# Performance work log

Hardware: AMD Instinct MI355X
Metric: run time of the kernel (lower is better)

## Reference

```python
import jax, jax.numpy as jnp
import numpy as np

H = 1024
V = 50257
L = 512


def setup_inputs() -> dict:
    key = jax.random.key(0)
    ks = jax.random.split(key, 12)
    s = 0.02
    return {
        "input_tok": jax.random.randint(ks[0], (1,), 0, V, dtype=jnp.int64),
        "hidden": jax.random.normal(ks[1], (1, 1, H), dtype=jnp.float32),
        "encoder_outputs": jax.random.normal(ks[2], (L, 1, H), dtype=jnp.float32),
        "embedding_w": jax.random.normal(ks[3], (V, H), dtype=jnp.float32) * s,
        "attn_combine_w": jax.random.normal(ks[4], (H, 2 * H), dtype=jnp.float32) * s,
        "attn_combine_b": jax.random.normal(ks[5], (H,), dtype=jnp.float32) * s,
        "w_ih": jax.random.normal(ks[6], (3 * H, H), dtype=jnp.float32) * s,
        "w_hh": jax.random.normal(ks[7], (3 * H, H), dtype=jnp.float32) * s,
        "b_ih": jax.random.normal(ks[8], (3 * H,), dtype=jnp.float32) * s,
        "b_hh": jax.random.normal(ks[9], (3 * H,), dtype=jnp.float32) * s,
        "out_w": jax.random.normal(ks[10], (V, H), dtype=jnp.float32) * s,
        "out_b": jax.random.normal(ks[11], (V,), dtype=jnp.float32) * s,
    }


def reference(input_tok, hidden, encoder_outputs, embedding_w,
              attn_combine_w, attn_combine_b, w_ih, w_hh, b_ih, b_hh,
              out_w, out_b):
    # embedding(input).view(1,1,-1); dropout is identity in eval mode
    embedded = embedding_w[input_tok[0]][None, :]          # [1, H]
    enc = encoder_outputs[:, 0, :]                          # [L, H]
    h0 = hidden[0]                                          # [1, H]
    # dot-product attention: hidden[0] @ enc^T
    attn_weights = jax.nn.softmax(h0 @ enc.T, axis=1)      # [1, L]
    attn_applied = attn_weights @ enc                       # [1, H]
    combined = jnp.concatenate([embedded, attn_applied], axis=1)  # [1, 2H]
    x = jax.nn.relu(combined @ attn_combine_w.T + attn_combine_b)  # [1, H]
    # single-step GRU cell (PyTorch gate ordering: r, z, n)
    gi = x @ w_ih.T + b_ih                                  # [1, 3H]
    gh = h0 @ w_hh.T + b_hh                                 # [1, 3H]
    r = jax.nn.sigmoid(gi[:, :H] + gh[:, :H])
    z = jax.nn.sigmoid(gi[:, H:2 * H] + gh[:, H:2 * H])
    n = jnp.tanh(gi[:, 2 * H:] + r * gh[:, 2 * H:])
    h_new = (1.0 - z) * n + z * h0                          # [1, H]
    logp = jax.nn.log_softmax(h_new @ out_w.T + out_b, axis=1)  # [1, V]
    return logp, h_new[None], attn_weights
```

## Files before the change

### kernel.cpp

```cpp
#include <hip/hip_runtime.h>
#include <math.h>

#define H  1024
#define H2 2048
#define H3 3072
#define V  50257
#define L  512

__device__ __forceinline__ float dot4(float4 a, float4 b) {
    return a.x*b.x + a.y*b.y + a.z*b.z + a.w*b.w;
}
__device__ __forceinline__ float wave_red_sum(float acc) {
    for (int off = 32; off > 0; off >>= 1) acc += __shfl_down(acc, off, 64);
    return acc;
}

__global__ void __launch_bounds__(256) k_pre(
        const float* __restrict__ h0, const float* __restrict__ enc,
        const float* __restrict__ w_hh, const float* __restrict__ b_hh,
        float* __restrict__ scores, float* __restrict__ gh) {
    __shared__ float s[4];
    int t = threadIdx.x, lane = t & 63, wv = t >> 6;
    if (blockIdx.x < 512) {
        int l = blockIdx.x;
        float4 a = ((const float4*)(enc + (size_t)l * H))[t];
        float4 b = ((const float4*)h0)[t];
        float acc = wave_red_sum(dot4(a, b));
        if (lane == 0) s[wv] = acc;
        __syncthreads();
        if (t == 0) scores[l] = s[0] + s[1] + s[2] + s[3];
    } else {
        int row = (blockIdx.x - 512) * 4 + wv;
        const float4* wr = (const float4*)(w_hh + (size_t)row * H);
        const float4* h4 = (const float4*)h0;
        float acc = 0.f;
        #pragma unroll
        for (int j = 0; j < 4; ++j) acc += dot4(wr[j * 64 + lane], h4[j * 64 + lane]);
        acc = wave_red_sum(acc);
        if (lane == 0) gh[row] = acc + b_hh[row];
    }
}

__global__ void __launch_bounds__(256) k_softmax_attn(
        const float* __restrict__ enc, const float* __restrict__ scores,
        float* __restrict__ attn_applied, float* __restrict__ d_out) {
    __shared__ float wl[L];
    __shared__ float red[256];
    __shared__ float part[8][32];
    int t = threadIdx.x;
    float s0 = scores[t], s1 = scores[t + 256];
    red[t] = fmaxf(s0, s1);
    __syncthreads();
    for (int off = 128; off > 0; off >>= 1) {
        if (t < off) red[t] = fmaxf(red[t], red[t + off]);
        __syncthreads();
    }
    float gmax = red[0];
    __syncthreads();
    float e0 = expf(s0 - gmax), e1 = expf(s1 - gmax);
    red[t] = e0 + e1;
    __syncthreads();
    for (int off = 128; off > 0; off >>= 1) {
        if (t < off) red[t] += red[t + off];
        __syncthreads();
    }
    float inv = 1.0f / red[0];
    wl[t]       = e0 * inv;
    wl[t + 256] = e1 * inv;
    __syncthreads();
    if (blockIdx.x == 0) {
        d_out[V + H + t]       = wl[t];
        d_out[V + H + t + 256] = wl[t + 256];
    }
    int c = t & 31, sIdx = t >> 5;
    int col = blockIdx.x * 32 + c;
    float acc = 0.f;
    for (int l = sIdx * 64; l < sIdx * 64 + 64; ++l)
        acc += wl[l] * enc[(size_t)l * H + col];
    part[sIdx][c] = acc;
    __syncthreads();
    if (sIdx == 0) {
        float sum = 0.f;
        #pragma unroll
        for (int k = 0; k < 8; ++k) sum += part[k][c];
        attn_applied[col] = sum;
    }
}

__global__ void __launch_bounds__(256) k_combine(
        const float* __restrict__ emb_w, const int* __restrict__ tok,
        const float* __restrict__ attn_applied, const float* __restrict__ Wc,
        const float* __restrict__ bc, float* __restrict__ x) {
    __shared__ float comb[H2];
    int t = threadIdx.x;
    int tk = tok[0];
    ((float4*)comb)[t]       = ((const float4*)(emb_w + (size_t)tk * H))[t];
    ((float4*)comb)[t + 256] = ((const float4*)attn_applied)[t];
    __syncthreads();
    int lane = t & 63, wv = t >> 6;
    int row = blockIdx.x * 4 + wv;
    const float4* wr = (const float4*)(Wc + (size_t)row * H2);
    float acc = 0.f;
    #pragma unroll
    for (int j = 0; j < 8; ++j) acc += dot4(wr[j * 64 + lane], ((const float4*)comb)[j * 64 + lane]);
    acc = wave_red_sum(acc);
    if (lane == 0) x[row] = fmaxf(acc + bc[row], 0.f);
}

__global__ void __launch_bounds__(256) k_gi_gru(
        const float* __restrict__ x, const float* __restrict__ h0,
        const float* __restrict__ w_ih, const float* __restrict__ b_ih,
        const float* __restrict__ gh, float* __restrict__ d_out,
        float* __restrict__ hnew) {
    int t = threadIdx.x, lane = t & 63, wv = t >> 6;
    int i = blockIdx.x * 4 + wv;
    const float4* xv = (const float4*)x;
    float g[3];
    #pragma unroll
    for (int k = 0; k < 3; ++k) {
        const float4* wr = (const float4*)(w_ih + (size_t)(k * H + i) * H);
        float acc = 0.f;
        #pragma unroll
        for (int j = 0; j < 4; ++j) acc += dot4(wr[j * 64 + lane], xv[j * 64 + lane]);
        g[k] = wave_red_sum(acc);
    }
    if (lane == 0) {
        float gir = g[0] + b_ih[i];
        float giz = g[1] + b_ih[H + i];
        float gin = g[2] + b_ih[2 * H + i];
        float r = 1.f / (1.f + expf(-(gir + gh[i])));
        float z = 1.f / (1.f + expf(-(giz + gh[H + i])));
        float n = tanhf(gin + r * gh[2 * H + i]);
        float h = (1.f - z) * n + z * h0[i];
        d_out[V + i] = h;
        hnew[i] = h;
    }
}

__global__ void __launch_bounds__(256) k_logits(
        const float* __restrict__ hnew, const float* __restrict__ out_w,
        const float* __restrict__ out_b, float* __restrict__ logits) {
    __shared__ float hs[H];
    int t = threadIdx.x;
    ((float4*)hs)[t] = ((const float4*)hnew)[t];
    __syncthreads();
    int lane = t & 63, wv = t >> 6;
    int row0 = (blockIdx.x * 4 + wv) * 2;
    if (row0 >= V) return;
    const float4* hs4 = (const float4*)hs;
    const float4* w0 = (const float4*)(out_w + (size_t)row0 * H);
    float acc0 = 0.f, acc1 = 0.f;
    if (row0 + 1 < V) {
        const float4* w1 = (const float4*)(out_w + (size_t)(row0 + 1) * H);
        #pragma unroll
        for (int j = 0; j < 4; ++j) {
            float4 b = hs4[j * 64 + lane];
            acc0 += dot4(w0[j * 64 + lane], b);
            acc1 += dot4(w1[j * 64 + lane], b);
        }
        for (int off = 32; off > 0; off >>= 1) {
            acc0 += __shfl_down(acc0, off, 64);
            acc1 += __shfl_down(acc1, off, 64);
        }
        if (lane == 0) {
            logits[row0]     = acc0 + out_b[row0];
            logits[row0 + 1] = acc1 + out_b[row0 + 1];
        }
    } else {
        #pragma unroll
        for (int j = 0; j < 4; ++j) acc0 += dot4(w0[j * 64 + lane], hs4[j * 64 + lane]);
        acc0 = wave_red_sum(acc0);
        if (lane == 0) logits[row0] = acc0 + out_b[row0];
    }
}

__global__ void __launch_bounds__(256) k_lse_part(
        const float* __restrict__ logits, float* __restrict__ pm,
        float* __restrict__ ps) {
    __shared__ float red[4];
    int b = blockIdx.x, t = threadIdx.x, lane = t & 63, wv = t >> 6;
    const int CH = (V + 63) / 64;
    int begin = b * CH;
    int end = begin + CH; if (end > V) end = V;
    float v[4]; int cnt = 0;
    for (int i = begin + t; i < end; i += 256) v[cnt++] = logits[i];
    float m = -INFINITY;
    for (int c = 0; c < cnt; ++c) m = fmaxf(m, v[c]);
    for (int off = 32; off > 0; off >>= 1) m = fmaxf(m, __shfl_down(m, off, 64));
    if (lane == 0) red[wv] = m;
    __syncthreads();
    float M = fmaxf(fmaxf(red[0], red[1]), fmaxf(red[2], red[3]));
    __syncthreads();
    float s = 0.f;
    for (int c = 0; c < cnt; ++c) s += expf(v[c] - M);
    s = wave_red_sum(s);
    if (lane == 0) red[wv] = s;
    __syncthreads();
    if (t == 0) {
        pm[b] = M;
        ps[b] = red[0] + red[1] + red[2] + red[3];
    }
}

__global__ void __launch_bounds__(256) k_logp(
        float* __restrict__ d_out, const float* __restrict__ pm,
        const float* __restrict__ ps) {
    __shared__ float sh[2];
    int t = threadIdx.x;
    if (t < 64) {
        float m = pm[t], s = ps[t];
        float M = m;
        for (int off = 32; off > 0; off >>= 1) M = fmaxf(M, __shfl_down(M, off, 64));
        M = __shfl(M, 0, 64);
        float sc = s * expf(m - M);
        sc = wave_red_sum(sc);
        if (t == 0) { sh[0] = M; sh[1] = logf(sc); }
    }
    __syncthreads();
    float M = sh[0], Ls = sh[1];
    int i = blockIdx.x * 256 + t;
    if (i < V) d_out[i] = d_out[i] - M - Ls;
}

extern "C" void kernel_launch(void* const* d_in, const int* in_sizes, int n_in,
                              void* d_out, int out_size, void* d_ws, size_t ws_size,
                              hipStream_t stream) {
    const int*   tok    = (const int*)d_in[0];
    const float* hidden = (const float*)d_in[1];
    const float* enc    = (const float*)d_in[2];
    const float* emb_w  = (const float*)d_in[3];
    const float* Wc     = (const float*)d_in[4];
    const float* bc     = (const float*)d_in[5];
    const float* w_ih   = (const float*)d_in[6];
    const float* w_hh   = (const float*)d_in[7];
    const float* b_ih   = (const float*)d_in[8];
    const float* b_hh   = (const float*)d_in[9];
    const float* out_w  = (const float*)d_in[10];
    const float* out_b  = (const float*)d_in[11];
    float* out = (float*)d_out;
    float* ws  = (float*)d_ws;

    float* scores       = ws;
    float* gh           = ws + 1024;
    float* attn_applied = ws + 4096;
    float* xbuf         = ws + 5120;
    float* hnew         = ws + 6144;
    float* pm           = ws + 7168;
    float* psum         = ws + 7232;

    k_pre         <<<1280, 256, 0, stream>>>(hidden, enc, w_hh, b_hh, scores, gh);
    k_softmax_attn<<<32,   256, 0, stream>>>(enc, scores, attn_applied, out);
    k_combine     <<<256,  256, 0, stream>>>(emb_w, tok, attn_applied, Wc, bc, xbuf);
    k_gi_gru      <<<256,  256, 0, stream>>>(xbuf, hidden, w_ih, b_ih, gh, out, hnew);
    k_logits      <<<(V + 7) / 8, 256, 0, stream>>>(hnew, out_w, out_b, out);
    k_lse_part    <<<64,   256, 0, stream>>>(out, pm, psum);
    k_logp        <<<(V + 255) / 256, 256, 0, stream>>>(out, pm, psum);
}
```

Before: 416.8 us.

## Fuse decoder step into one cooperative kernel with grid syncs and online logsumexp

Replaces the seven separate launches with a single cooperative kernel of 1024 blocks. The stages (scores and gh, softmax-attention, combine, GRU, logits, log-softmax) are separated by grid.sync() calls. Attention application is rewritten so each block reduces one column across all rows, and the logits stage folds the running max and sum into an online logsumexp, which removes the separate pass over the logits. The aim is to cut launch gaps and an extra read of the logits, at the price of five grid-wide barriers and fewer waves resident per CU during the large out_w GEMV.

```diff
diff --git a/kernel.cpp b/kernel.cpp
--- a/kernel.cpp
+++ b/kernel.cpp
@@ -1,225 +1,228 @@
 #include <hip/hip_runtime.h>
+#include <hip/hip_cooperative_groups.h>
 #include <math.h>
+
+namespace cg = cooperative_groups;
 
 #define H  1024
 #define H2 2048
-#define H3 3072
 #define V  50257
 #define L  512
+#define NB 1024
+#define NT 256
+#define NG ((V + 7) / 8)
 
 __device__ __forceinline__ float dot4(float4 a, float4 b) {
     return a.x*b.x + a.y*b.y + a.z*b.z + a.w*b.w;
 }
-__device__ __forceinline__ float wave_red_sum(float acc) {
-    for (int off = 32; off > 0; off >>= 1) acc += __shfl_down(acc, off, 64);
-    return acc;
-}
-
-__global__ void __launch_bounds__(256) k_pre(
-        const float* __restrict__ h0, const float* __restrict__ enc,
-        const float* __restrict__ w_hh, const float* __restrict__ b_hh,
-        float* __restrict__ scores, float* __restrict__ gh) {
-    __shared__ float s[4];
-    int t = threadIdx.x, lane = t & 63, wv = t >> 6;
-    if (blockIdx.x < 512) {
-        int l = blockIdx.x;
-        float4 a = ((const float4*)(enc + (size_t)l * H))[t];
-        float4 b = ((const float4*)h0)[t];
-        float acc = wave_red_sum(dot4(a, b));
-        if (lane == 0) s[wv] = acc;
-        __syncthreads();
-        if (t == 0) scores[l] = s[0] + s[1] + s[2] + s[3];
-    } else {
-        int row = (blockIdx.x - 512) * 4 + wv;
-        const float4* wr = (const float4*)(w_hh + (size_t)row * H);
-        const float4* h4 = (const float4*)h0;
-        float acc = 0.f;
+__device__ __forceinline__ float wave_red_sum(float v) {
+    #pragma unroll
+    for (int off = 32; off > 0; off >>= 1) v += __shfl_down(v, off, 64);
+    return v;
+}
+__device__ __forceinline__ float wave_red_max(float v) {
+    #pragma unroll
+    for (int off = 32; off > 0; off >>= 1) v = fmaxf(v, __shfl_down(v, off, 64));
+    return v;
+}
+
+__global__ void __launch_bounds__(NT, 4) k_fused(
+        const int* __restrict__ tok,   const float* __restrict__ h0,
+        const float* __restrict__ enc, const float* __restrict__ emb_w,
+        const float* __restrict__ Wc,  const float* __restrict__ bc,
+        const float* __restrict__ w_ih,const float* __restrict__ w_hh,
+        const float* __restrict__ b_ih,const float* __restrict__ b_hh,
+        const float* __restrict__ out_w,const float* __restrict__ out_b,
+        float* __restrict__ d_out,     float* __restrict__ ws)
+{
+    cg::grid_group grid = cg::this_grid();
+    __shared__ float4 sh4[512];
+    __shared__ float  sred[8];
+
+    float* scores = ws;
+    float* gh     = ws + 1024;
+    float* attn   = ws + 4096;
+    float* xv     = ws + 5120;
+    float* hnew   = ws + 6144;
+    float* pm     = ws + 7168;
+    float* ps     = ws + 8192;
+
+    const int t = threadIdx.x, lane = t & 63, wv = t >> 6;
+    const int b = blockIdx.x;
+
+    for (int it = b; it < 512 + 768; it += NB) {
+        if (it < 512) {
+            const float4* er = (const float4*)(enc + (size_t)it * H);
+            float acc = wave_red_sum(dot4(er[t], ((const float4*)h0)[t]));
+            if (lane == 0) sred[wv] = acc;
+            __syncthreads();
+            if (t == 0) scores[it] = sred[0] + sred[1] + sred[2] + sred[3];
+            __syncthreads();
+        } else {
+            int row = (it - 512) * 4 + wv;
+            const float4* wr = (const float4*)(w_hh + (size_t)row * H);
+            const float4* h4 = (const float4*)h0;
+            float acc = 0.f;
+            #pragma unroll
+            for (int j = 0; j < 4; ++j) acc += dot4(wr[j*64 + lane], h4[j*64 + lane]);
+            acc = wave_red_sum(acc);
+            if (lane == 0) gh[row] = acc + b_hh[row];
+        }
+    }
+    grid.sync();
+
+    {
+        float s0 = scores[t], s1 = scores[t + 256];
+        float m = wave_red_max(fmaxf(s0, s1));
+        if (lane == 0) sred[wv] = m;
+        __syncthreads();
+        float gmax = fmaxf(fmaxf(sred[0], sred[1]), fmaxf(sred[2], sred[3]));
+        __syncthreads();
+        float e0 = expf(s0 - gmax), e1 = expf(s1 - gmax);
+        float ssum = wave_red_sum(e0 + e1);
+        if (lane == 0) sred[wv] = ssum;
+        __syncthreads();
+        float inv = 1.f / (sred[0] + sred[1] + sred[2] + sred[3]);
+        __syncthreads();
+        float w0 = e0 * inv, w1 = e1 * inv;
+        if (b == 0) {
+            d_out[V + H + t]       = w0;
+            d_out[V + H + 256 + t] = w1;
+        }
+        float acc = w0 * enc[(size_t)t * H + b] + w1 * enc[(size_t)(t + 256) * H + b];
+        acc = wave_red_sum(acc);
+        if (lane == 0) sred[wv] = acc;
+        __syncthreads();
+        if (t == 0) attn[b] = sred[0] + sred[1] + sred[2] + sred[3];
+    }
+    grid.sync();
+
+    {
+        int tk = tok[0];
+        const float4* er = (const float4*)(emb_w + (size_t)tk * H);
+        sh4[t]       = er[t];
+        sh4[256 + t] = ((const float4*)attn)[t];
+        __syncthreads();
+        const float4* wr = (const float4*)(Wc + (size_t)b * H2);
+        float acc = dot4(wr[t], sh4[t]) + dot4(wr[256 + t], sh4[256 + t]);
+        acc = wave_red_sum(acc);
+        if (lane == 0) sred[wv] = acc;
+        __syncthreads();
+        if (t == 0) xv[b] = fmaxf(sred[0] + sred[1] + sred[2] + sred[3] + bc[b], 0.f);
+        __syncthreads();
+    }
+    grid.sync();
+
+    {
+        if (wv < 3) {
+            const float4* wr = (const float4*)(w_ih + (size_t)(wv * H + b) * H);
+            const float4* x4 = (const float4*)xv;
+            float acc = 0.f;
+            #pragma unroll
+            for (int j = 0; j < 4; ++j) acc += dot4(wr[j*64 + lane], x4[j*64 + lane]);
+            acc = wave_red_sum(acc);
+            if (lane == 0) sred[wv] = acc;
+        }
+        __syncthreads();
+        if (t == 0) {
+            float gir = sred[0] + b_ih[b];
+            float giz = sred[1] + b_ih[H + b];
+            float gin = sred[2] + b_ih[2 * H + b];
+            float r = 1.f / (1.f + expf(-(gir + gh[b])));
+            float z = 1.f / (1.f + expf(-(giz + gh[H + b])));
+            float n = tanhf(gin + r * gh[2 * H + b]);
+            float h = (1.f - z) * n + z * h0[b];
+            hnew[b] = h;
+            d_out[V + b] = h;
+        }
+    }
+    grid.sync();
+
+    {
+        sh4[t] = ((const float4*)hnew)[t];
+        __syncthreads();
+        float m_run = -INFINITY, s_run = 0.f;
+        for (int g = b; g < NG; g += NB) {
+            int r0 = g * 8 + wv * 2;
+            if (r0 + 1 < V) {
+                const float4* w0 = (const float4*)(out_w + (size_t)r0 * H);
+                const float4* w1 = w0 + 256;
+                float a0 = 0.f, a1 = 0.f;
+                #pragma unroll
+                for (int j = 0; j < 4; ++j) {
+                    float4 hv = sh4[j*64 + lane];
+                    a0 += dot4(w0[j*64 + lane], hv);
+                    a1 += dot4(w1[j*64 + lane], hv);
+                }
+                #pragma unroll
+                for (int off = 32; off > 0; off >>= 1) {
+                    a0 += __shfl_down(a0, off, 64);
+                    a1 += __shfl_down(a1, off, 64);
+                }
+                if (lane == 0) {
+                    float v0 = a0 + out_b[r0];
+                    float v1 = a1 + out_b[r0 + 1];
+                    d_out[r0]     = v0;
+                    d_out[r0 + 1] = v1;
+                    float mn = fmaxf(m_run, fmaxf(v0, v1));
+                    s_run = s_run * expf(m_run - mn) + expf(v0 - mn) + expf(v1 - mn);
+                    m_run = mn;
+                }
+            } else if (r0 < V) {
+                const float4* w0 = (const float4*)(out_w + (size_t)r0 * H);
+                float a0 = 0.f;
+                #pragma unroll
+                for (int j = 0; j < 4; ++j) a0 += dot4(w0[j*64 + lane], sh4[j*64 + lane]);
+                a0 = wave_red_sum(a0);
+                if (lane == 0) {
+                    float v0 = a0 + out_b[r0];
+                    d_out[r0] = v0;
+                    float mn = fmaxf(m_run, v0);
+                    s_run = s_run * expf(m_run - mn) + expf(v0 - mn);
+                    m_run = mn;
+                }
+            }
+        }
+        if (lane == 0) { sred[wv] = m_run; sred[4 + wv] = s_run; }
+        __syncthreads();
+        if (t == 0) {
+            float M = fmaxf(fmaxf(sred[0], sred[1]), fmaxf(sred[2], sred[3]));
+            float S = 0.f;
+            #pragma unroll
+            for (int k = 0; k < 4; ++k) S += sred[4 + k] * expf(sred[k] - M);
+            pm[b] = M; ps[b] = S;
+        }
+    }
+    grid.sync();
+
+    {
+        float m = -INFINITY, s = 0.f;
         #pragma unroll
-        for (int j = 0; j < 4; ++j) acc += dot4(wr[j * 64 + lane], h4[j * 64 + lane]);
-        acc = wave_red_sum(acc);
-        if (lane == 0) gh[row] = acc + b_hh[row];
-    }
-}
-
-__global__ void __launch_bounds__(256) k_softmax_attn(
-        const float* __restrict__ enc, const float* __restrict__ scores,
-        float* __restrict__ attn_applied, float* __restrict__ d_out) {
-    __shared__ float wl[L];
-    __shared__ float red[256];
-    __shared__ float part[8][32];
-    int t = threadIdx.x;
-    float s0 = scores[t], s1 = scores[t + 256];
-    red[t] = fmaxf(s0, s1);
-    __syncthreads();
-    for (int off = 128; off > 0; off >>= 1) {
-        if (t < off) red[t] = fmaxf(red[t], red[t + off]);
-        __syncthreads();
-    }
-    float gmax = red[0];
-    __syncthreads();
-    float e0 = expf(s0 - gmax), e1 = expf(s1 - gmax);
-    red[t] = e0 + e1;
-    __syncthreads();
-    for (int off = 128; off > 0; off >>= 1) {
-        if (t < off) red[t] += red[t + off];
-        __syncthreads();
-    }
-    float inv = 1.0f / red[0];
-    wl[t]       = e0 * inv;
-    wl[t + 256] = e1 * inv;
-    __syncthreads();
-    if (blockIdx.x == 0) {
-        d_out[V + H + t]       = wl[t];
-        d_out[V + H + t + 256] = wl[t + 256];
-    }
-    int c = t & 31, sIdx = t >> 5;
-    int col = blockIdx.x * 32 + c;
-    float acc = 0.f;
-    for (int l = sIdx * 64; l < sIdx * 64 + 64; ++l)
-        acc += wl[l] * enc[(size_t)l * H + col];
-    part[sIdx][c] = acc;
-    __syncthreads();
-    if (sIdx == 0) {
-        float sum = 0.f;
+        for (int k = 0; k < 4; ++k) {
+            int i = t * 4 + k;
+            float mi = pm[i], si = ps[i];
+            float mn = fmaxf(m, mi);
+            s = s * expf(m - mn) + si * expf(mi - mn);
+            m = mn;
+        }
         #pragma unroll
-        for (int k = 0; k < 8; ++k) sum += part[k][c];
-        attn_applied[col] = sum;
-    }
-}
-
-__global__ void __launch_bounds__(256) k_combine(
-        const float* __restrict__ emb_w, const int* __restrict__ tok,
-        const float* __restrict__ attn_applied, const float* __restrict__ Wc,
-        const float* __restrict__ bc, float* __restrict__ x) {
-    __shared__ float comb[H2];
-    int t = threadIdx.x;
-    int tk = tok[0];
-    ((float4*)comb)[t]       = ((const float4*)(emb_w + (size_t)tk * H))[t];
-    ((float4*)comb)[t + 256] = ((const float4*)attn_applied)[t];
-    __syncthreads();
-    int lane = t & 63, wv = t >> 6;
-    int row = blockIdx.x * 4 + wv;
-    const float4* wr = (const float4*)(Wc + (size_t)row * H2);
-    float acc = 0.f;
-    #pragma unroll
-    for (int j = 0; j < 8; ++j) acc += dot4(wr[j * 64 + lane], ((const float4*)comb)[j * 64 + lane]);
-    acc = wave_red_sum(acc);
-    if (lane == 0) x[row] = fmaxf(acc + bc[row], 0.f);
-}
-
-__global__ void __launch_bounds__(256) k_gi_gru(
-        const float* __restrict__ x, const float* __restrict__ h0,
-        const float* __restrict__ w_ih, const float* __restrict__ b_ih,
-        const float* __restrict__ gh, float* __restrict__ d_out,
-        float* __restrict__ hnew) {
-    int t = threadIdx.x, lane = t & 63, wv = t >> 6;
-    int i = blockIdx.x * 4 + wv;
-    const float4* xv = (const float4*)x;
-    float g[3];
-    #pragma unroll
-    for (int k = 0; k < 3; ++k) {
-        const float4* wr = (const float4*)(w_ih + (size_t)(k * H + i) * H);
-        float acc = 0.f;
+        for (int off = 32; off > 0; off >>= 1) {
+            float mo = __shfl_down(m, off, 64);
+            float so = __shfl_down(s, off, 64);
+            float mn = fmaxf(m, mo);
+            s = s * expf(m - mn) + so * expf(mo - mn);
+            m = mn;
+        }
+        if (lane == 0) { sred[wv] = m; sred[4 + wv] = s; }
+        __syncthreads();
+        float M = fmaxf(fmaxf(sred[0], sred[1]), fmaxf(sred[2], sred[3]));
+        float S = 0.f;
         #pragma unroll
-        for (int j = 0; j < 4; ++j) acc += dot4(wr[j * 64 + lane], xv[j * 64 + lane]);
-        g[k] = wave_red_sum(acc);
-    }
-    if (lane == 0) {
-        float gir = g[0] + b_ih[i];
-        float giz = g[1] + b_ih[H + i];
-        float gin = g[2] + b_ih[2 * H + i];
-        float r = 1.f / (1.f + expf(-(gir + gh[i])));
-        float z = 1.f / (1.f + expf(-(giz + gh[H + i])));
-        float n = tanhf(gin + r * gh[2 * H + i]);
-        float h = (1.f - z) * n + z * h0[i];
-        d_out[V + i] = h;
-        hnew[i] = h;
-    }
-}
-
-__global__ void __launch_bounds__(256) k_logits(
-        const float* __restrict__ hnew, const float* __restrict__ out_w,
-        const float* __restrict__ out_b, float* __restrict__ logits) {
-    __shared__ float hs[H];
-    int t = threadIdx.x;
-    ((float4*)hs)[t] = ((const float4*)hnew)[t];
-    __syncthreads();
-    int lane = t & 63, wv = t >> 6;
-    int row0 = (blockIdx.x * 4 + wv) * 2;
-    if (row0 >= V) return;
-    const float4* hs4 = (const float4*)hs;
-    const float4* w0 = (const float4*)(out_w + (size_t)row0 * H);
-    float acc0 = 0.f, acc1 = 0.f;
-    if (row0 + 1 < V) {
-        const float4* w1 = (const float4*)(out_w + (size_t)(row0 + 1) * H);
-        #pragma unroll
-        for (int j = 0; j < 4; ++j) {
-            float4 b = hs4[j * 64 + lane];
-            acc0 += dot4(w0[j * 64 + lane], b);
-            acc1 += dot4(w1[j * 64 + lane], b);
-        }
-        for (int off = 32; off > 0; off >>= 1) {
-            acc0 += __shfl_down(acc0, off, 64);
-            acc1 += __shfl_down(acc1, off, 64);
-        }
-        if (lane == 0) {
-            logits[row0]     = acc0 + out_b[row0];
-            logits[row0 + 1] = acc1 + out_b[row0 + 1];
-        }
-    } else {
-        #pragma unroll
-        for (int j = 0; j < 4; ++j) acc0 += dot4(w0[j * 64 + lane], hs4[j * 64 + lane]);
-        acc0 = wave_red_sum(acc0);
-        if (lane == 0) logits[row0] = acc0 + out_b[row0];
-    }
-}
-
-__global__ void __launch_bounds__(256) k_lse_part(
-        const float* __restrict__ logits, float* __restrict__ pm,
-        float* __restrict__ ps) {
-    __shared__ float red[4];
-    int b = blockIdx.x, t = threadIdx.x, lane = t & 63, wv = t >> 6;
-    const int CH = (V + 63) / 64;
-    int begin = b * CH;
-    int end = begin + CH; if (end > V) end = V;
-    float v[4]; int cnt = 0;
-    for (int i = begin + t; i < end; i += 256) v[cnt++] = logits[i];
-    float m = -INFINITY;
-    for (int c = 0; c < cnt; ++c) m = fmaxf(m, v[c]);
-    for (int off = 32; off > 0; off >>= 1) m = fmaxf(m, __shfl_down(m, off, 64));
-    if (lane == 0) red[wv] = m;
-    __syncthreads();
-    float M = fmaxf(fmaxf(red[0], red[1]), fmaxf(red[2], red[3]));
-    __syncthreads();
-    float s = 0.f;
-    for (int c = 0; c < cnt; ++c) s += expf(v[c] - M);
-    s = wave_red_sum(s);
-    if (lane == 0) red[wv] = s;
-    __syncthreads();
-    if (t == 0) {
-        pm[b] = M;
-        ps[b] = red[0] + red[1] + red[2] + red[3];
-    }
-}
-
-__global__ void __launch_bounds__(256) k_logp(
-        float* __restrict__ d_out, const float* __restrict__ pm,
-        const float* __restrict__ ps) {
-    __shared__ float sh[2];
-    int t = threadIdx.x;
-    if (t < 64) {
-        float m = pm[t], s = ps[t];
-        float M = m;
-        for (int off = 32; off > 0; off >>= 1) M = fmaxf(M, __shfl_down(M, off, 64));
-        M = __shfl(M, 0, 64);
-        float sc = s * expf(m - M);
-        sc = wave_red_sum(sc);
-        if (t == 0) { sh[0] = M; sh[1] = logf(sc); }
-    }
-    __syncthreads();
-    float M = sh[0], Ls = sh[1];
-    int i = blockIdx.x * 256 + t;
-    if (i < V) d_out[i] = d_out[i] - M - Ls;
+        for (int k = 0; k < 4; ++k) S += sred[4 + k] * expf(sred[k] - M);
+        float off = M + logf(S);
+        int i = b * NT + t;
+        if (i < V) d_out[i] -= off;
+    }
 }
 
 extern "C" void kernel_launch(void* const* d_in, const int* in_sizes, int n_in,
@@ -240,19 +243,9 @@
     float* out = (float*)d_out;
     float* ws  = (float*)d_ws;
 
-    float* scores       = ws;
-    float* gh           = ws + 1024;
-    float* attn_applied = ws + 4096;
-    float* xbuf         = ws + 5120;
-    float* hnew         = ws + 6144;
-    float* pm           = ws + 7168;
-    float* psum         = ws + 7232;
-
-    k_pre         <<<1280, 256, 0, stream>>>(hidden, enc, w_hh, b_hh, scores, gh);
-    k_softmax_attn<<<32,   256, 0, stream>>>(enc, scores, attn_applied, out);
-    k_combine     <<<256,  256, 0, stream>>>(emb_w, tok, attn_applied, Wc, bc, xbuf);
-    k_gi_gru      <<<256,  256, 0, stream>>>(xbuf, hidden, w_ih, b_ih, gh, out, hnew);
-    k_logits      <<<(V + 7) / 8, 256, 0, stream>>>(hnew, out_w, out_b, out);
-    k_lse_part    <<<64,   256, 0, stream>>>(out, pm, psum);
-    k_logp        <<<(V + 255) / 256, 256, 0, stream>>>(out, pm, psum);
-}
+    void* args[] = { &tok, &hidden, &enc, &emb_w, &Wc, &bc,
+                     &w_ih, &w_hh, &b_ih, &b_hh, &out_w, &out_b,
+                     &out, &ws };
+    hipLaunchCooperativeKernel((const void*)k_fused, dim3(NB), dim3(NT),
+                               args, 0, stream);
+}
```

After: 966.4 us. +131.9%, slower.
